# Optimization experiments

Measured on AMD Instinct MI355X. Metric: run time of the kernel, lower is better.

The kernel has to match this reference:

```python
import jax, jax.numpy as jnp
import numpy as np

ROTARY_DIM = 64
ROPE_THETA = 10000.0
BLOCK_SIZE = 24


def setup_inputs() -> dict:
    key = jax.random.key(0)
    ks = jax.random.split(key, 6)
    B, T_code = 2, 2048
    d_cond, d_code, d_spk, d_model, vocab = 512, 512, 192, 1024, 6561
    cond = jax.random.normal(ks[0], (B, 1, d_cond), dtype=jnp.float32)
    spk = jax.random.normal(ks[1], (B, 1, d_spk), dtype=jnp.float32)
    code = jax.random.randint(ks[2], (B, T_code), 0, vocab, dtype=jnp.int64)
    embed_table = jax.random.normal(ks[3], (vocab, d_code), dtype=jnp.float32)
    W = jax.random.normal(ks[4], (d_cond + d_code + d_spk, d_model), dtype=jnp.float32) * 0.02
    b = jax.random.normal(ks[5], (d_model,), dtype=jnp.float32) * 0.02
    return {"cond": cond, "spk": spk, "code": code,
            "embed_table": embed_table, "W": W, "b": b}


def _rope(T):
    # DitRotary.forward
    pos = jnp.arange(T, dtype=jnp.float32).reshape(-1, 1)          # [T,1]
    theta = 1.0 / ROPE_THETA ** (jnp.arange(0, ROTARY_DIM, 2, dtype=jnp.float32) / ROTARY_DIM)
    idx = pos * theta                                              # [T,32]
    r = jnp.stack([jnp.cos(idx), jnp.sin(idx)])                    # [2,T,32]
    r = jnp.stack((r, r), axis=-1).reshape(2, T, ROTARY_DIM)       # [2,T,64]
    return r[:, None, :, None, :]                                  # [2,1,T,1,64]


def reference(cond, spk, code, embed_table, W, b):
    B, T_code = code.shape
    T = T_code * 2  # max_duration
    d_cond = cond.shape[-1]
    d_code = embed_table.shape[-1]
    code_embed = jnp.repeat(embed_table[code], 2, axis=1)          # [B,T,d_code]
    # concat([cond.repeat, code_embed, spk.repeat]) @ W + b, computed as split
    # matmuls with broadcast (same math, avoids materializing repeats)
    W_cond = W[:d_cond]
    W_code = W[d_cond:d_cond + d_code]
    W_spk = W[d_cond + d_code:]
    code_embeds = (jnp.einsum('btc,cd->btd', code_embed, W_code)
                   + cond @ W_cond + spk @ W_spk + b)              # [B,T,d_model]
    rope = _rope(T)
    # block-causal mask precompute
    blk = jnp.arange(T) // BLOCK_SIZE
    mask = (blk[None, :] - blk[:, None]).reshape(1, 1, T, T)       # int
    return code_embeds, rope, mask
```

## Files before the change

### kernel.cpp

```cpp
#include <hip/hip_runtime.h>
#include <hip/hip_bf16.h>
#include <cstdint>

typedef short short8 __attribute__((ext_vector_type(8)));
typedef float f32x4 __attribute__((ext_vector_type(4)));

#define OUT0_SZ  (2*4096*1024)
#define OUT1_OFF OUT0_SZ
#define OUT1_SZ  (2*4096*64)
#define OUT2_OFF (OUT0_SZ + OUT1_SZ)

__device__ __forceinline__ unsigned short f2bf(float f) {
    unsigned u = __float_as_uint(f);
    unsigned r = (u + 0x7FFFu + ((u >> 16) & 1u)) >> 16;
    return (unsigned short)r;
}

__global__ __launch_bounds__(256) void bias_kernel(
    const float* __restrict__ cond, const float* __restrict__ spk,
    const float* __restrict__ W, const float* __restrict__ bvec,
    float* __restrict__ bias)
{
    __shared__ float red[8][32];
    const int b  = blockIdx.x >> 5;
    const int d0 = (blockIdx.x & 31) * 32;
    const int dl = threadIdx.x & 31;
    const int ks = threadIdx.x >> 5;
    const int d  = d0 + dl;
    const float* condb = cond + b * 512;
    const float* spkb  = spk + b * 192;
    float acc = 0.f;
    #pragma unroll 8
    for (int i = 0; i < 64; ++i) {
        int k = ks * 64 + i;
        acc = fmaf(condb[k], W[(size_t)k * 1024 + d], acc);
    }
    #pragma unroll 8
    for (int i = 0; i < 24; ++i) {
        int s = ks * 24 + i;
        acc = fmaf(spkb[s], W[(size_t)(1024 + s) * 1024 + d], acc);
    }
    red[ks][dl] = acc;
    __syncthreads();
    if (ks == 0) {
        float t = acc + bvec[d];
        #pragma unroll
        for (int j = 1; j < 8; ++j) t += red[j][dl];
        bias[b * 1024 + d] = t;
    }
}

__global__ __launch_bounds__(256) void gather_kernel(
    const float* __restrict__ embed, const int* __restrict__ code,
    unsigned short* __restrict__ Ag)
{
    int gtid = blockIdx.x * 256 + threadIdx.x;
    int r = gtid >> 6;
    int c = (gtid & 63) * 8;
    int cv = code[r];
    const float* s = embed + (size_t)cv * 512 + c;
    float4 f0 = *(const float4*)s;
    float4 f1 = *(const float4*)(s + 4);
    short8 v;
    v[0] = (short)f2bf(f0.x); v[1] = (short)f2bf(f0.y);
    v[2] = (short)f2bf(f0.z); v[3] = (short)f2bf(f0.w);
    v[4] = (short)f2bf(f1.x); v[5] = (short)f2bf(f1.y);
    v[6] = (short)f2bf(f1.z); v[7] = (short)f2bf(f1.w);
    *(short8*)&Ag[(size_t)r * 512 + c] = v;
}

__global__ __launch_bounds__(256) void transpose_kernel(
    const float* __restrict__ W, unsigned short* __restrict__ Wt)
{
    __shared__ float tile[32][33];
    int k0 = blockIdx.x * 32;
    int n0 = blockIdx.y * 32;
    int lx = threadIdx.x & 31;
    int ly = threadIdx.x >> 5;
    #pragma unroll
    for (int rr = 0; rr < 32; rr += 8)
        tile[ly + rr][lx] = W[(size_t)(512 + k0 + ly + rr) * 1024 + n0 + lx];
    __syncthreads();
    #pragma unroll
    for (int rr = 0; rr < 32; rr += 8)
        Wt[(size_t)(n0 + ly + rr) * 512 + k0 + lx] = f2bf(tile[lx][ly + rr]);
}

__global__ __launch_bounds__(256) void rope_mask_kernel(
    float* __restrict__ out1, float* __restrict__ out2)
{
    int tid = blockIdx.x * 256 + threadIdx.x;
    if (tid < 262144) {
        int kk = tid & 31;
        int t  = (tid >> 5) & 4095;
        int c  = tid >> 17;
        double theta = exp2(-(double)kk * 0.41524101186092028);
        double a = (double)t * theta;
        float vf = (float)(c ? sin(a) : cos(a));
        float2 w; w.x = vf; w.y = vf;
        *(float2*)&out1[(size_t)(c * 4096 + t) * 64 + kk * 2] = w;
    } else {
        int q = tid - 262144;
        int i = q >> 10;
        int j = (q & 1023) << 2;
        int bi = i / 24;
        float4 v;
        v.x = (float)((j    ) / 24 - bi);
        v.y = (float)((j + 1) / 24 - bi);
        v.z = (float)((j + 2) / 24 - bi);
        v.w = (float)((j + 3) / 24 - bi);
        ((float4*)out2)[q] = v;
    }
}

__global__ __launch_bounds__(256) void gemm_kernel(
    const unsigned short* __restrict__ Ag, const unsigned short* __restrict__ Wt,
    const float* __restrict__ bias, float* __restrict__ out0)
{
    __shared__ short8 AsV[128 * 64 / 8];
    __shared__ short8 BsV[128 * 64 / 8];
    unsigned short* As = (unsigned short*)AsV;
    unsigned short* Bs = (unsigned short*)BsV;

    const int tid = threadIdx.x;
    const int bm = blockIdx.x;
    const int bn = blockIdx.y;
    const int lane = tid & 63;
    const int wid = tid >> 6;
    const int wr = wid >> 1;
    const int wc = wid & 1;
    const int l15 = lane & 15;
    const int l4  = lane >> 4;

    f32x4 acc[4][4];
    #pragma unroll
    for (int i = 0; i < 4; ++i)
        #pragma unroll
        for (int j = 0; j < 4; ++j)
            acc[i][j] = (f32x4){0.f, 0.f, 0.f, 0.f};

    long a_off[4]; long b_off[4]; int dst[4];
    #pragma unroll
    for (int i = 0; i < 4; ++i) {
        int ch = i * 256 + tid;
        int r  = ch >> 3;
        int kc = (ch & 7) * 8;
        a_off[i] = (long)(bm * 128 + r) * 512 + kc;
        b_off[i] = (long)(bn * 128 + r) * 512 + kc;
        dst[i]   = r * 64 + (kc ^ ((r & 7) << 3));
    }

    for (int kt = 0; kt < 512; kt += 64) {
        __syncthreads();
        #pragma unroll
        for (int i = 0; i < 4; ++i)
            *(short8*)&As[dst[i]] = *(const short8*)&Ag[a_off[i] + kt];
        #pragma unroll
        for (int i = 0; i < 4; ++i)
            *(short8*)&Bs[dst[i]] = *(const short8*)&Wt[b_off[i] + kt];
        __syncthreads();
        #pragma unroll
        for (int ks = 0; ks < 2; ++ks) {
            const int kb = ks * 32 + l4 * 8;
            short8 af[4], bf[4];
            #pragma unroll
            for (int mi = 0; mi < 4; ++mi) {
                int r = wr * 64 + mi * 16 + l15;
                af[mi] = *(const short8*)&As[r * 64 + (kb ^ ((r & 7) << 3))];
            }
            #pragma unroll
            for (int ni = 0; ni < 4; ++ni) {
                int n = wc * 64 + ni * 16 + l15;
                bf[ni] = *(const short8*)&Bs[n * 64 + (kb ^ ((n & 7) << 3))];
            }
            #pragma unroll
            for (int mi = 0; mi < 4; ++mi)
                #pragma unroll
                for (int ni = 0; ni < 4; ++ni)
                    acc[mi][ni] = __builtin_amdgcn_mfma_f32_16x16x32_bf16(
                        af[mi], bf[ni], acc[mi][ni], 0, 0, 0);
        }
    }

    const int b = bm >> 4;
    const float* biasb = bias + b * 1024;
    #pragma unroll
    for (int ni = 0; ni < 4; ++ni) {
        const int n = bn * 128 + wc * 64 + ni * 16 + l15;
        const float bv = biasb[n];
        #pragma unroll
        for (int mi = 0; mi < 4; ++mi) {
            const int mbase = bm * 128 + wr * 64 + mi * 16 + l4 * 4;
            #pragma unroll
            for (int j = 0; j < 4; ++j) {
                const int u = (mbase + j) & 2047;
                const size_t o = ((size_t)(b * 4096 + 2 * u)) * 1024 + n;
                const float v = acc[mi][ni][j] + bv;
                out0[o] = v;
                out0[o + 1024] = v;
            }
        }
    }
}

extern "C" void kernel_launch(void* const* d_in, const int* in_sizes, int n_in,
                              void* d_out, int out_size, void* d_ws, size_t ws_size,
                              hipStream_t stream) {
    const float* cond  = (const float*)d_in[0];
    const float* spk   = (const float*)d_in[1];
    const int*   code  = (const int*)d_in[2];
    const float* embed = (const float*)d_in[3];
    const float* W     = (const float*)d_in[4];
    const float* bvec  = (const float*)d_in[5];

    float* out  = (float*)d_out;
    float* out0 = out;
    float* out1 = out + OUT1_OFF;
    float* out2 = out + OUT2_OFF;

    float* bias = (float*)d_ws;
    unsigned short* Wt = (unsigned short*)((char*)d_ws + 8192);
    unsigned short* Ag = (unsigned short*)((char*)d_ws + 8192 + 1048576);

    gather_kernel<<<1024, 256, 0, stream>>>(embed, code, Ag);
    bias_kernel<<<64, 256, 0, stream>>>(cond, spk, W, bvec, bias);
    transpose_kernel<<<dim3(16, 32), 256, 0, stream>>>(W, Wt);
    rope_mask_kernel<<<17408, 256, 0, stream>>>(out1, out2);
    gemm_kernel<<<dim3(32, 8), 256, 0, stream>>>(Ag, Wt, bias, out0);
}
```

Measured before the change: 151.2 us.

## Merge five launches into prep and main kernels with block-range dispatch

Combines gather, transpose and bias into one prep kernel, and GEMM, rope and mask generation into one main kernel, with each block choosing its role from its block index. The mask section now writes four float4 per thread, so it needs fewer blocks. This cuts launch overhead and lets the memory-bound rope/mask writes run alongside the GEMM blocks. In exchange, the main kernel reserves the GEMM's shared memory for every block, which can lower occupancy for the simple write blocks.

Result: slower. 155.4 us (+2.8%).

```diff
diff --git a/kernel.cpp b/kernel.cpp
--- a/kernel.cpp
+++ b/kernel.cpp
@@ -7,8 +7,7 @@
 
 #define OUT0_SZ  (2*4096*1024)
 #define OUT1_OFF OUT0_SZ
-#define OUT1_SZ  (2*4096*64)
-#define OUT2_OFF (OUT0_SZ + OUT1_SZ)
+#define OUT2_OFF (OUT0_SZ + 2*4096*64)
 
 __device__ __forceinline__ unsigned short f2bf(float f) {
     unsigned u = __float_as_uint(f);
@@ -16,81 +15,168 @@
     return (unsigned short)r;
 }
 
-__global__ __launch_bounds__(256) void bias_kernel(
+__global__ __launch_bounds__(256) void prep_kernel(
+    const float* __restrict__ embed, const int* __restrict__ code,
     const float* __restrict__ cond, const float* __restrict__ spk,
     const float* __restrict__ W, const float* __restrict__ bvec,
+    unsigned short* __restrict__ Ag, unsigned short* __restrict__ Wt,
     float* __restrict__ bias)
 {
+    __shared__ float tile[32][33];
     __shared__ float red[8][32];
-    const int b  = blockIdx.x >> 5;
-    const int d0 = (blockIdx.x & 31) * 32;
-    const int dl = threadIdx.x & 31;
-    const int ks = threadIdx.x >> 5;
-    const int d  = d0 + dl;
-    const float* condb = cond + b * 512;
-    const float* spkb  = spk + b * 192;
-    float acc = 0.f;
-    #pragma unroll 8
-    for (int i = 0; i < 64; ++i) {
-        int k = ks * 64 + i;
-        acc = fmaf(condb[k], W[(size_t)k * 1024 + d], acc);
+    const int bid = blockIdx.x;
+
+    if (bid < 1024) {
+        int gtid = bid * 256 + threadIdx.x;
+        int r = gtid >> 6;
+        int c = (gtid & 63) * 8;
+        int cv = code[r];
+        const float* s = embed + (size_t)cv * 512 + c;
+        float4 f0 = *(const float4*)s;
+        float4 f1 = *(const float4*)(s + 4);
+        short8 v;
+        v[0] = (short)f2bf(f0.x); v[1] = (short)f2bf(f0.y);
+        v[2] = (short)f2bf(f0.z); v[3] = (short)f2bf(f0.w);
+        v[4] = (short)f2bf(f1.x); v[5] = (short)f2bf(f1.y);
+        v[6] = (short)f2bf(f1.z); v[7] = (short)f2bf(f1.w);
+        *(short8*)&Ag[(size_t)r * 512 + c] = v;
+    } else if (bid < 1536) {
+        int idx = bid - 1024;
+        int k0 = (idx & 15) * 32;
+        int n0 = (idx >> 4) * 32;
+        int lx = threadIdx.x & 31;
+        int ly = threadIdx.x >> 5;
+        #pragma unroll
+        for (int rr = 0; rr < 32; rr += 8)
+            tile[ly + rr][lx] = W[(size_t)(512 + k0 + ly + rr) * 1024 + n0 + lx];
+        __syncthreads();
+        #pragma unroll
+        for (int rr = 0; rr < 32; rr += 8)
+            Wt[(size_t)(n0 + ly + rr) * 512 + k0 + lx] = f2bf(tile[lx][ly + rr]);
+    } else {
+        int idx = bid - 1536;
+        const int b  = idx >> 5;
+        const int d0 = (idx & 31) * 32;
+        const int dl = threadIdx.x & 31;
+        const int ks = threadIdx.x >> 5;
+        const int d  = d0 + dl;
+        const float* condb = cond + b * 512;
+        const float* spkb  = spk + b * 192;
+        float acc = 0.f;
+        #pragma unroll 8
+        for (int i = 0; i < 64; ++i) {
+            int k = ks * 64 + i;
+            acc = fmaf(condb[k], W[(size_t)k * 1024 + d], acc);
+        }
+        #pragma unroll 8
+        for (int i = 0; i < 24; ++i) {
+            int s = ks * 24 + i;
+            acc = fmaf(spkb[s], W[(size_t)(1024 + s) * 1024 + d], acc);
+        }
+        red[ks][dl] = acc;
+        __syncthreads();
+        if (ks == 0) {
+            float t = acc + bvec[d];
+            #pragma unroll
+            for (int j = 1; j < 8; ++j) t += red[j][dl];
+            bias[b * 1024 + d] = t;
+        }
     }
-    #pragma unroll 8
-    for (int i = 0; i < 24; ++i) {
-        int s = ks * 24 + i;
-        acc = fmaf(spkb[s], W[(size_t)(1024 + s) * 1024 + d], acc);
-    }
-    red[ks][dl] = acc;
-    __syncthreads();
-    if (ks == 0) {
-        float t = acc + bvec[d];
-        #pragma unroll
-        for (int j = 1; j < 8; ++j) t += red[j][dl];
-        bias[b * 1024 + d] = t;
-    }
-}
-
-__global__ __launch_bounds__(256) void gather_kernel(
-    const float* __restrict__ embed, const int* __restrict__ code,
-    unsigned short* __restrict__ Ag)
-{
-    int gtid = blockIdx.x * 256 + threadIdx.x;
-    int r = gtid >> 6;
-    int c = (gtid & 63) * 8;
-    int cv = code[r];
-    const float* s = embed + (size_t)cv * 512 + c;
-    float4 f0 = *(const float4*)s;
-    float4 f1 = *(const float4*)(s + 4);
-    short8 v;
-    v[0] = (short)f2bf(f0.x); v[1] = (short)f2bf(f0.y);
-    v[2] = (short)f2bf(f0.z); v[3] = (short)f2bf(f0.w);
-    v[4] = (short)f2bf(f1.x); v[5] = (short)f2bf(f1.y);
-    v[6] = (short)f2bf(f1.z); v[7] = (short)f2bf(f1.w);
-    *(short8*)&Ag[(size_t)r * 512 + c] = v;
-}
-
-__global__ __launch_bounds__(256) void transpose_kernel(
-    const float* __restrict__ W, unsigned short* __restrict__ Wt)
-{
-    __shared__ float tile[32][33];
-    int k0 = blockIdx.x * 32;
-    int n0 = blockIdx.y * 32;
-    int lx = threadIdx.x & 31;
-    int ly = threadIdx.x >> 5;
-    #pragma unroll
-    for (int rr = 0; rr < 32; rr += 8)
-        tile[ly + rr][lx] = W[(size_t)(512 + k0 + ly + rr) * 1024 + n0 + lx];
-    __syncthreads();
-    #pragma unroll
-    for (int rr = 0; rr < 32; rr += 8)
-        Wt[(size_t)(n0 + ly + rr) * 512 + k0 + lx] = f2bf(tile[lx][ly + rr]);
-}
-
-__global__ __launch_bounds__(256) void rope_mask_kernel(
+}
+
+__global__ __launch_bounds__(256) void main_kernel(
+    const unsigned short* __restrict__ Ag, const unsigned short* __restrict__ Wt,
+    const float* __restrict__ bias, float* __restrict__ out0,
     float* __restrict__ out1, float* __restrict__ out2)
 {
-    int tid = blockIdx.x * 256 + threadIdx.x;
-    if (tid < 262144) {
+    __shared__ short8 AsV[128 * 64 / 8];
+    __shared__ short8 BsV[128 * 64 / 8];
+    const int bid = blockIdx.x;
+
+    if (bid < 256) {
+        unsigned short* As = (unsigned short*)AsV;
+        unsigned short* Bs = (unsigned short*)BsV;
+        const int tid = threadIdx.x;
+        const int bm = bid >> 3;
+        const int bn = bid & 7;
+        const int lane = tid & 63;
+        const int wid = tid >> 6;
+        const int wr = wid >> 1;
+        const int wc = wid & 1;
+        const int l15 = lane & 15;
+        const int l4  = lane >> 4;
+
+        f32x4 acc[4][4];
+        #pragma unroll
+        for (int i = 0; i < 4; ++i)
+            #pragma unroll
+            for (int j = 0; j < 4; ++j)
+                acc[i][j] = (f32x4){0.f, 0.f, 0.f, 0.f};
+
+        long a_off[4]; long b_off[4]; int dst[4];
+        #pragma unroll
+        for (int i = 0; i < 4; ++i) {
+            int ch = i * 256 + tid;
+            int r  = ch >> 3;
+            int kc = (ch & 7) * 8;
+            a_off[i] = (long)(bm * 128 + r) * 512 + kc;
+            b_off[i] = (long)(bn * 128 + r) * 512 + kc;
+            dst[i]   = r * 64 + (kc ^ ((r & 7) << 3));
+        }
+
+        for (int kt = 0; kt < 512; kt += 64) {
+            __syncthreads();
+            #pragma unroll
+            for (int i = 0; i < 4; ++i)
+                *(short8*)&As[dst[i]] = *(const short8*)&Ag[a_off[i] + kt];
+            #pragma unroll
+            for (int i = 0; i < 4; ++i)
+                *(short8*)&Bs[dst[i]] = *(const short8*)&Wt[b_off[i] + kt];
+            __syncthreads();
+            #pragma unroll
+            for (int ks = 0; ks < 2; ++ks) {
+                const int kb = ks * 32 + l4 * 8;
+                short8 af[4], bf[4];
+                #pragma unroll
+                for (int mi = 0; mi < 4; ++mi) {
+                    int r = wr * 64 + mi * 16 + l15;
+                    af[mi] = *(const short8*)&As[r * 64 + (kb ^ ((r & 7) << 3))];
+                }
+                #pragma unroll
+                for (int ni = 0; ni < 4; ++ni) {
+                    int n = wc * 64 + ni * 16 + l15;
+                    bf[ni] = *(const short8*)&Bs[n * 64 + (kb ^ ((n & 7) << 3))];
+                }
+                #pragma unroll
+                for (int mi = 0; mi < 4; ++mi)
+                    #pragma unroll
+                    for (int ni = 0; ni < 4; ++ni)
+                        acc[mi][ni] = __builtin_amdgcn_mfma_f32_16x16x32_bf16(
+                            af[mi], bf[ni], acc[mi][ni], 0, 0, 0);
+            }
+        }
+
+        const int b = bm >> 4;
+        const float* biasb = bias + b * 1024;
+        #pragma unroll
+        for (int ni = 0; ni < 4; ++ni) {
+            const int n = bn * 128 + wc * 64 + ni * 16 + l15;
+            const float bv = biasb[n];
+            #pragma unroll
+            for (int mi = 0; mi < 4; ++mi) {
+                const int mbase = bm * 128 + wr * 64 + mi * 16 + l4 * 4;
+                #pragma unroll
+                for (int j = 0; j < 4; ++j) {
+                    const int u = (mbase + j) & 2047;
+                    const size_t o = ((size_t)(b * 4096 + 2 * u)) * 1024 + n;
+                    const float v = acc[mi][ni][j] + bv;
+                    out0[o] = v;
+                    out0[o + 1024] = v;
+                }
+            }
+        }
+    } else if (bid < 1280) {
+        int tid = (bid - 256) * 256 + threadIdx.x;
         int kk = tid & 31;
         int t  = (tid >> 5) & 4095;
         int c  = tid >> 17;
@@ -100,105 +186,19 @@
         float2 w; w.x = vf; w.y = vf;
         *(float2*)&out1[(size_t)(c * 4096 + t) * 64 + kk * 2] = w;
     } else {
-        int q = tid - 262144;
-        int i = q >> 10;
-        int j = (q & 1023) << 2;
-        int bi = i / 24;
-        float4 v;
-        v.x = (float)((j    ) / 24 - bi);
-        v.y = (float)((j + 1) / 24 - bi);
-        v.z = (float)((j + 2) / 24 - bi);
-        v.w = (float)((j + 3) / 24 - bi);
-        ((float4*)out2)[q] = v;
-    }
-}
-
-__global__ __launch_bounds__(256) void gemm_kernel(
-    const unsigned short* __restrict__ Ag, const unsigned short* __restrict__ Wt,
-    const float* __restrict__ bias, float* __restrict__ out0)
-{
-    __shared__ short8 AsV[128 * 64 / 8];
-    __shared__ short8 BsV[128 * 64 / 8];
-    unsigned short* As = (unsigned short*)AsV;
-    unsigned short* Bs = (unsigned short*)BsV;
-
-    const int tid = threadIdx.x;
-    const int bm = blockIdx.x;
-    const int bn = blockIdx.y;
-    const int lane = tid & 63;
-    const int wid = tid >> 6;
-    const int wr = wid >> 1;
-    const int wc = wid & 1;
-    const int l15 = lane & 15;
-    const int l4  = lane >> 4;
-
-    f32x4 acc[4][4];
-    #pragma unroll
-    for (int i = 0; i < 4; ++i)
-        #pragma unroll
-        for (int j = 0; j < 4; ++j)
-            acc[i][j] = (f32x4){0.f, 0.f, 0.f, 0.f};
-
-    long a_off[4]; long b_off[4]; int dst[4];
-    #pragma unroll
-    for (int i = 0; i < 4; ++i) {
-        int ch = i * 256 + tid;
-        int r  = ch >> 3;
-        int kc = (ch & 7) * 8;
-        a_off[i] = (long)(bm * 128 + r) * 512 + kc;
-        b_off[i] = (long)(bn * 128 + r) * 512 + kc;
-        dst[i]   = r * 64 + (kc ^ ((r & 7) << 3));
-    }
-
-    for (int kt = 0; kt < 512; kt += 64) {
-        __syncthreads();
-        #pragma unroll
-        for (int i = 0; i < 4; ++i)
-            *(short8*)&As[dst[i]] = *(const short8*)&Ag[a_off[i] + kt];
-        #pragma unroll
-        for (int i = 0; i < 4; ++i)
-            *(short8*)&Bs[dst[i]] = *(const short8*)&Wt[b_off[i] + kt];
-        __syncthreads();
-        #pragma unroll
-        for (int ks = 0; ks < 2; ++ks) {
-            const int kb = ks * 32 + l4 * 8;
-            short8 af[4], bf[4];
-            #pragma unroll
-            for (int mi = 0; mi < 4; ++mi) {
-                int r = wr * 64 + mi * 16 + l15;
-                af[mi] = *(const short8*)&As[r * 64 + (kb ^ ((r & 7) << 3))];
-            }
-            #pragma unroll
-            for (int ni = 0; ni < 4; ++ni) {
-                int n = wc * 64 + ni * 16 + l15;
-                bf[ni] = *(const short8*)&Bs[n * 64 + (kb ^ ((n & 7) << 3))];
-            }
-            #pragma unroll
-            for (int mi = 0; mi < 4; ++mi)
-                #pragma unroll
-                for (int ni = 0; ni < 4; ++ni)
-                    acc[mi][ni] = __builtin_amdgcn_mfma_f32_16x16x32_bf16(
-                        af[mi], bf[ni], acc[mi][ni], 0, 0, 0);
-        }
-    }
-
-    const int b = bm >> 4;
-    const float* biasb = bias + b * 1024;
-    #pragma unroll
-    for (int ni = 0; ni < 4; ++ni) {
-        const int n = bn * 128 + wc * 64 + ni * 16 + l15;
-        const float bv = biasb[n];
-        #pragma unroll
-        for (int mi = 0; mi < 4; ++mi) {
-            const int mbase = bm * 128 + wr * 64 + mi * 16 + l4 * 4;
-            #pragma unroll
-            for (int j = 0; j < 4; ++j) {
-                const int u = (mbase + j) & 2047;
-                const size_t o = ((size_t)(b * 4096 + 2 * u)) * 1024 + n;
-                const float v = acc[mi][ni][j] + bv;
-                out0[o] = v;
-                out0[o + 1024] = v;
-            }
+        int q0 = (bid - 1280) * 1024 + threadIdx.x * 4;
+        #pragma unroll
+        for (int s = 0; s < 4; ++s) {
+            int q = q0 + s;
+            int i = q >> 10;
+            int j = (q & 1023) << 2;
+            int bi = i / 24;
+            float4 v;
+            v.x = (float)((j    ) / 24 - bi);
+            v.y = (float)((j + 1) / 24 - bi);
+            v.z = (float)((j + 2) / 24 - bi);
+            v.w = (float)((j + 3) / 24 - bi);
+            ((float4*)out2)[q] = v;
         }
     }
 }
@@ -222,9 +222,7 @@
     unsigned short* Wt = (unsigned short*)((char*)d_ws + 8192);
     unsigned short* Ag = (unsigned short*)((char*)d_ws + 8192 + 1048576);
 
-    gather_kernel<<<1024, 256, 0, stream>>>(embed, code, Ag);
-    bias_kernel<<<64, 256, 0, stream>>>(cond, spk, W, bvec, bias);
-    transpose_kernel<<<dim3(16, 32), 256, 0, stream>>>(W, Wt);
-    rope_mask_kernel<<<17408, 256, 0, stream>>>(out1, out2);
-    gemm_kernel<<<dim3(32, 8), 256, 0, stream>>>(Ag, Wt, bias, out0);
-}
+    prep_kernel<<<1600, 256, 0, stream>>>(embed, code, cond, spk, W, bvec,
+                                          Ag, Wt, bias);
+    main_kernel<<<5376, 256, 0, stream>>>(Ag, Wt, bias, out0, out1, out2);
+}
```
